# Optimization experiments

Hardware: AMD Instinct MI355X
Metric: run time of the kernel (lower is better)

## Reference

```python
import math
import jax, jax.numpy as jnp
from jax import lax
import numpy as np

D_MODEL, D_STATE, D_CONV, EXPAND = 96, 16, 3, 2
D_INNER = EXPAND * D_MODEL            # 192
DT_RANK = math.ceil(D_MODEL / 16)     # 6
B_, H_, W_ = 2, 64, 64


def setup_inputs() -> dict:
    key = jax.random.key(0)
    ks = jax.random.split(key, 8)
    x = jax.random.normal(ks[0], (B_, H_, W_, D_MODEL), jnp.float32)
    in_proj_w = jax.random.normal(ks[1], (2 * D_INNER, D_MODEL), jnp.float32) * (D_MODEL ** -0.5)
    conv_w = jax.random.normal(ks[2], (D_INNER, 1, D_CONV, D_CONV), jnp.float32) * 0.1  # depthwise OIHW
    conv_b = jax.random.normal(ks[3], (D_INNER,), jnp.float32) * 0.1
    x_proj_weight = jax.random.normal(ks[4], (4, DT_RANK + 2 * D_STATE, D_INNER), jnp.float32) * (D_INNER ** -0.5)
    dt_init_std = DT_RANK ** -0.5
    dt_projs_weight = jax.random.uniform(ks[5], (4, D_INNER, DT_RANK), jnp.float32, -dt_init_std, dt_init_std)
    dt = jnp.exp(jax.random.uniform(ks[6], (4, D_INNER), jnp.float32) * (math.log(0.1) - math.log(0.001)) + math.log(0.001))
    dt = jnp.clip(dt, 1e-4, None)
    dt_projs_bias = dt + jnp.log(-jnp.expm1(-dt))  # inverse softplus init
    A_logs = jnp.log(jnp.tile(jnp.arange(1.0, D_STATE + 1.0, dtype=jnp.float32), (4 * D_INNER, 1)))  # (4*D, N)
    Ds = jnp.ones((4 * D_INNER,), jnp.float32)
    out_norm_w = jnp.ones((D_INNER,), jnp.float32)
    out_norm_b = jnp.zeros((D_INNER,), jnp.float32)
    out_proj_w = jax.random.normal(ks[7], (D_MODEL, D_INNER), jnp.float32) * (D_INNER ** -0.5)
    return dict(x=x, in_proj_w=in_proj_w, conv_w=conv_w, conv_b=conv_b,
                x_proj_weight=x_proj_weight, dt_projs_weight=dt_projs_weight,
                dt_projs_bias=dt_projs_bias, A_logs=A_logs, Ds=Ds,
                out_norm_w=out_norm_w, out_norm_b=out_norm_b, out_proj_w=out_proj_w)


def _ss2d(x, in_proj_w, conv_w, conv_b, x_proj_weight, dt_projs_weight,
          dt_projs_bias, A_logs, Ds, out_norm_w, out_norm_b, out_proj_w):
    B, H, W, C = x.shape
    K = 4
    d_inner = conv_w.shape[0]
    d_state = A_logs.shape[1]
    dt_rank = dt_projs_weight.shape[2]
    L = H * W

    # in_proj + split into x / gate z
    xz = jnp.einsum('bhwc,ec->bhwe', x, in_proj_w)
    xi, z = jnp.split(xz, 2, axis=-1)

    # depthwise 3x3 conv (padding=1) + SiLU, channels-first
    xc = jnp.transpose(xi, (0, 3, 1, 2))  # B,D,H,W
    xc = lax.conv_general_dilated(xc, conv_w, (1, 1), 'SAME',
                                  feature_group_count=d_inner,
                                  dimension_numbers=('NCHW', 'OIHW', 'NCHW'))
    xc = jax.nn.silu(xc + conv_b[None, :, None, None])

    # 4 scan directions: row-major, col-major, and their reverses
    x_hw = xc.reshape(B, d_inner, L)
    x_wh = jnp.transpose(xc, (0, 1, 3, 2)).reshape(B, d_inner, L)
    x_hwwh = jnp.stack([x_hw, x_wh], axis=1)                        # B,2,D,L
    xs = jnp.concatenate([x_hwwh, jnp.flip(x_hwwh, axis=-1)], axis=1)  # B,K,D,L

    x_dbl = jnp.einsum('bkdl,kcd->bkcl', xs, x_proj_weight)
    dts, Bs, Cs = jnp.split(x_dbl, [dt_rank, dt_rank + d_state], axis=2)
    dts = jnp.einsum('bkrl,kdr->bkdl', dts, dt_projs_weight)
    delta = jax.nn.softplus(dts + dt_projs_bias[None, :, :, None])  # B,K,D,L
    A = -jnp.exp(A_logs).reshape(K, d_inner, d_state)               # K,D,N

    # selective scan over L (serial recurrence)
    d_s = jnp.moveaxis(delta, -1, 0)  # L,B,K,D
    u_s = jnp.moveaxis(xs, -1, 0)     # L,B,K,D
    B_s = jnp.moveaxis(Bs, -1, 0)     # L,B,K,N
    C_s = jnp.moveaxis(Cs, -1, 0)     # L,B,K,N

    def step(h, inp):
        d_t, u_t, Bt, Ct = inp
        dA = jnp.exp(d_t[..., None] * A)                       # B,K,D,N
        h = h * dA + (d_t * u_t)[..., None] * Bt[:, :, None, :]
        y = jnp.einsum('bkdn,bkn->bkd', h, Ct)
        return h, y

    h0 = jnp.zeros((B, K, d_inner, d_state), jnp.float32)
    _, ys = lax.scan(step, h0, (d_s, u_s, B_s, C_s))  # ys: L,B,K,D
    ys = jnp.moveaxis(ys, 0, -1)                      # B,K,D,L
    out_y = ys + xs * Ds.reshape(K, d_inner)[None, :, :, None]

    # merge directions back to row-major layout
    inv_y = jnp.flip(out_y[:, 2:4], axis=-1)
    wh_y = jnp.transpose(out_y[:, 1].reshape(B, d_inner, W, H), (0, 1, 3, 2)).reshape(B, d_inner, L)
    invwh_y = jnp.transpose(inv_y[:, 1].reshape(B, d_inner, W, H), (0, 1, 3, 2)).reshape(B, d_inner, L)
    y = out_y[:, 0] + inv_y[:, 0] + wh_y + invwh_y    # B,D,L

    y = jnp.transpose(y, (0, 2, 1)).reshape(B, H, W, d_inner)
    mu = y.mean(-1, keepdims=True)
    var = y.var(-1, keepdims=True)
    y = (y - mu) * lax.rsqrt(var + 1e-5) * out_norm_w + out_norm_b
    y = y * jax.nn.silu(z)
    return jnp.einsum('bhwd,cd->bhwc', y, out_proj_w)


def reference(x, in_proj_w, conv_w, conv_b, x_proj_weight, dt_projs_weight,
              dt_projs_bias, A_logs, Ds, out_norm_w, out_norm_b, out_proj_w):
    return _ss2d(x, in_proj_w, conv_w, conv_b, x_proj_weight, dt_projs_weight,
                 dt_projs_bias, A_logs, Ds, out_norm_w, out_norm_b, out_proj_w)
```

## Files before the change

### kernel.cpp

```cpp
#include <hip/hip_runtime.h>
#include <math.h>

#define DMODEL 96
#define DIN    192
#define NST    16
#define RK     6
#define KDIR   4
#define LLEN   4096
#define BB     2
#define BP_TOT 8192
#define SCH    128
#define TCH    32

__global__ __launch_bounds__(192) void k_inproj(const float* __restrict__ x,
                                                const float* __restrict__ Wp,
                                                float* __restrict__ xi,
                                                float* __restrict__ z)
{
    __shared__ float xs[8 * 96];
    const int t  = threadIdx.x;
    const int p0 = blockIdx.x * 8;
    for (int idx = t; idx < 768; idx += 192)
        xs[idx] = x[(size_t)p0 * 96 + idx];
    __syncthreads();

    float acc0[8], acc1[8];
    #pragma unroll
    for (int i = 0; i < 8; ++i) { acc0[i] = 0.f; acc1[i] = 0.f; }
    const float* w0p = Wp + (size_t)t * 96;
    const float* w1p = Wp + (size_t)(t + 192) * 96;
    for (int k = 0; k < 96; k += 4) {
        float4 w0 = *(const float4*)(w0p + k);
        float4 w1 = *(const float4*)(w1p + k);
        #pragma unroll
        for (int p = 0; p < 8; ++p) {
            float4 xv = *(const float4*)&xs[p * 96 + k];
            acc0[p] = fmaf(w0.x, xv.x, fmaf(w0.y, xv.y, fmaf(w0.z, xv.z, fmaf(w0.w, xv.w, acc0[p]))));
            acc1[p] = fmaf(w1.x, xv.x, fmaf(w1.y, xv.y, fmaf(w1.z, xv.z, fmaf(w1.w, xv.w, acc1[p]))));
        }
    }
    #pragma unroll
    for (int p = 0; p < 8; ++p) {
        xi[(size_t)(p0 + p) * 192 + t] = acc0[p];
        z [(size_t)(p0 + p) * 192 + t] = acc1[p];
    }
}

__global__ __launch_bounds__(256) void k_conv(const float* __restrict__ xi,
                                              const float* __restrict__ cw,
                                              const float* __restrict__ cb,
                                              float* __restrict__ xc)
{
    int tid = blockIdx.x * 256 + threadIdx.x;
    int d  = tid % 192;
    int bp = tid / 192;
    int p  = bp & 4095;
    int b  = bp >> 12;
    int h  = p >> 6, w = p & 63;
    float s = cb[d];
    #pragma unroll
    for (int ky = 0; ky < 3; ++ky) {
        int hh = h + ky - 1;
        if (hh < 0 || hh >= 64) continue;
        #pragma unroll
        for (int kx = 0; kx < 3; ++kx) {
            int ww = w + kx - 1;
            if (ww < 0 || ww >= 64) continue;
            s += xi[((size_t)b * 4096 + hh * 64 + ww) * 192 + d] * cw[d * 9 + ky * 3 + kx];
        }
    }
    xc[tid] = s * (1.f / (1.f + __expf(-s)));
}

__device__ __forceinline__ int inv_perm(int kd, int p)
{
    if (kd == 0) return p;
    if (kd == 1) return ((p & 63) << 6) | (p >> 6);
    if (kd == 2) return 4095 - p;
    return 4095 - (((p & 63) << 6) | (p >> 6));
}

__device__ __forceinline__ int perm_pos(int k, int l)
{
    if (k == 0) return l;
    if (k == 1) return ((l & 63) << 6) | (l >> 6);
    if (k == 2) return 4095 - l;
    int lr = 4095 - l;
    return ((lr & 63) << 6) | (lr >> 6);
}

__device__ __forceinline__ float softplus_fast(float x)
{
    float r = __logf(1.f + __expf(x));
    return (x > 15.f) ? x : r;
}

__device__ __forceinline__ void pow_chain(float e1, float* aa)
{
    float e2 = e1 * e1, e4 = e2 * e2, e8 = e4 * e4, e16 = e8 * e8;
    float e3 = e2 * e1, e5 = e4 * e1, e6 = e4 * e2, e7 = e4 * e3;
    aa[0] = e1;  aa[1] = e2;  aa[2] = e3;  aa[3] = e4;
    aa[4] = e5;  aa[5] = e6;  aa[6] = e7;  aa[7] = e8;
    aa[8] = e8 * e1;  aa[9] = e8 * e2;  aa[10] = e8 * e3;  aa[11] = e8 * e4;
    aa[12] = e8 * e5; aa[13] = e8 * e6; aa[14] = e8 * e7;  aa[15] = e16;
}

__device__ __forceinline__ int sm_remap(int c)
{
    return (c < 6) ? (32 + c) : (c - 6);
}

__global__ __launch_bounds__(192) void k_xdbl(const float* __restrict__ xc,
                                              const float* __restrict__ xpw,
                                              float* __restrict__ xdk,
                                              float* __restrict__ y)
{
    __shared__ float xs[8 * 192];
    const int t  = threadIdx.x;
    const int p0 = blockIdx.x * 8;
    for (int idx = t; idx < 1536; idx += 192) {
        xs[idx] = xc[(size_t)p0 * 192 + idx];
        y[(size_t)p0 * 192 + idx] = 0.f;
    }
    __syncthreads();
    if (t >= 152) return;

    const int kd = t / 38, r = t % 38;
    float acc[8];
    #pragma unroll
    for (int i = 0; i < 8; ++i) acc[i] = 0.f;
    const float* wr = xpw + (size_t)t * 192;
    for (int k = 0; k < 192; k += 4) {
        float4 w = *(const float4*)(wr + k);
        #pragma unroll
        for (int p = 0; p < 8; ++p) {
            float4 xv = *(const float4*)&xs[p * 192 + k];
            acc[p] = fmaf(w.x, xv.x, fmaf(w.y, xv.y, fmaf(w.z, xv.z, fmaf(w.w, xv.w, acc[p]))));
        }
    }
    #pragma unroll
    for (int p = 0; p < 8; ++p) {
        int bp = p0 + p;
        int b  = bp >> 12, pp = bp & 4095;
        int l  = inv_perm(kd, pp);
        xdk[((size_t)(b * 4 + kd) * 4096 + l) * 38 + r] = acc[p];
    }
}

__global__ __launch_bounds__(192) void k_scan1(const float* __restrict__ xc,
                                               const float* __restrict__ xdk,
                                               const float* __restrict__ dtw,
                                               const float* __restrict__ dtb,
                                               const float* __restrict__ Alog,
                                               const float* __restrict__ Ds,
                                               float* __restrict__ hend,
                                               float* __restrict__ prodA,
                                               float* __restrict__ cdbuf,
                                               float* __restrict__ y)
{
    __shared__ float sm[TCH * 40];
    const int t   = threadIdx.x;
    const int blk = blockIdx.x;
    const int s = blk & (SCH - 1), k = (blk >> 7) & 3, b = blk >> 9;
    const int kd = k * 192 + t;
    const int l0 = s * TCH;

    const float* src = xdk + ((size_t)(b * 4 + k) * 4096 + l0) * 38;
    for (int idx = t; idx < TCH * 38; idx += 192) {
        int st = idx / 38, c = idx % 38;
        sm[st * 40 + sm_remap(c)] = src[idx];
    }

    const float A0 = -__expf(Alog[kd * 16]);
    bool fast = true;
    #pragma unroll
    for (int n = 1; n < 16; ++n) {
        float An = -__expf(Alog[kd * 16 + n]);
        fast = fast && (fabsf(An - (float)(n + 1) * A0) <= 1e-3f * fabsf(An));
    }
    float wdt[6];
    #pragma unroll
    for (int r = 0; r < 6; ++r) wdt[r] = dtw[kd * 6 + r];
    const float bias = dtb[kd];
    const float Dk   = Ds[kd];

    float h[16];
    #pragma unroll
    for (int n = 0; n < 16; ++n) h[n] = 0.f;
    float cd = 0.f;

    const float* xcb = xc + (size_t)b * 4096 * 192;
    float* yb = y + (size_t)b * 4096 * 192;
    int allfast = __syncthreads_and((int)fast);

    int p_cur = perm_pos(k, l0);
    float u = xcb[(size_t)p_cur * 192 + t];

    if (allfast) {
        for (int st = 0; st < TCH; ++st) {
            int p_next = (st + 1 < TCH) ? perm_pos(k, l0 + st + 1) : p_cur;
            float u_next = xcb[(size_t)p_next * 192 + t];
            const float* r = &sm[st * 40];
            float4 dq = *(const float4*)(r + 32);
            float xv = bias + dq.x * wdt[0] + dq.y * wdt[1] + dq.z * wdt[2]
                            + dq.w * wdt[3] + r[36] * wdt[4] + r[37] * wdt[5];
            float delta = softplus_fast(xv);
            cd += delta;
            cdbuf[((size_t)blk * TCH + st) * 192 + t] = cd;
            float du = delta * u;
            float aa[16];
            pow_chain(__expf(delta * A0), aa);
            float4 b0 = *(const float4*)(r),      b1 = *(const float4*)(r + 4);
            float4 b2 = *(const float4*)(r + 8),  b3 = *(const float4*)(r + 12);
            float4 c0 = *(const float4*)(r + 16), c1 = *(const float4*)(r + 20);
            float4 c2 = *(const float4*)(r + 24), c3 = *(const float4*)(r + 28);
            float bv[16] = {b0.x, b0.y, b0.z, b0.w, b1.x, b1.y, b1.z, b1.w,
                            b2.x, b2.y, b2.z, b2.w, b3.x, b3.y, b3.z, b3.w};
            float cv[16] = {c0.x, c0.y, c0.z, c0.w, c1.x, c1.y, c1.z, c1.w,
                            c2.x, c2.y, c2.z, c2.w, c3.x, c3.y, c3.z, c3.w};
            float acc = Dk * u;
            #pragma unroll
            for (int n = 0; n < 16; ++n) {
                h[n] = fmaf(h[n], aa[n], du * bv[n]);
                acc  = fmaf(h[n], cv[n], acc);
            }
            unsafeAtomicAdd(&yb[(size_t)p_cur * 192 + t], acc);
            u = u_next; p_cur = p_next;
        }
    } else {
        for (int st = 0; st < TCH; ++st) {
            int p_next = (st + 1 < TCH) ? perm_pos(k, l0 + st + 1) : p_cur;
            float u_next = xcb[(size_t)p_next * 192 + t];
            const float* r = &sm[st * 40];
            float xv = bias;
            #pragma unroll
            for (int j = 0; j < 6; ++j) xv += r[32 + j] * wdt[j];
            float delta = softplus_fast(xv);
            cd += delta;
            float du = delta * u;
            #pragma unroll
            for (int n = 0; n < 16; ++n) {
                float An = -__expf(Alog[kd * 16 + n]);
                h[n] = fmaf(h[n], __expf(delta * An), du * r[n]);
            }
            u = u_next; p_cur = p_next;
        }
    }

    size_t base = (size_t)blk * 3072 + t * 16;
    float ap[16];
    if (allfast) {
        pow_chain(__expf(cd * A0), ap);
    } else {
        #pragma unroll
        for (int n = 0; n < 16; ++n)
            ap[n] = __expf(-__expf(Alog[kd * 16 + n]) * cd);
    }
    #pragma unroll
    for (int i = 0; i < 4; ++i) {
        *(float4*)&hend [base + 4 * i] = make_float4(h[4*i], h[4*i+1], h[4*i+2], h[4*i+3]);
        *(float4*)&prodA[base + 4 * i] = make_float4(ap[4*i], ap[4*i+1], ap[4*i+2], ap[4*i+3]);
    }
}

__global__ __launch_bounds__(256) void k_scan2(const float* __restrict__ hend,
                                               float* __restrict__ prodA)
{
    int tid = blockIdx.x * 256 + threadIdx.x;
    int n  = tid & 15;
    int d  = (tid >> 4) % 192;
    int bk = tid / (192 * 16);
    size_t base = (size_t)bk * SCH * 3072 + d * 16 + n;
    float carry = 0.f;
    for (int s = 0; s < SCH; ++s) {
        size_t a = base + (size_t)s * 3072;
        float pa = prodA[a];
        float he = hend[a];
        prodA[a] = carry;
        carry = fmaf(pa, carry, he);
    }
}

__global__ __launch_bounds__(192) void k_scan3(const float* __restrict__ xc,
                                               const float* __restrict__ xdk,
                                               const float* __restrict__ dtw,
                                               const float* __restrict__ dtb,
                                               const float* __restrict__ Alog,
                                               const float* __restrict__ Ds,
                                               const float* __restrict__ hinit,
                                               const float* __restrict__ cdbuf,
                                               float* __restrict__ y)
{
    __shared__ float sm[TCH * 40];
    const int t   = threadIdx.x;
    const int blk = blockIdx.x;
    const int s = blk & (SCH - 1), k = (blk >> 7) & 3, b = blk >> 9;
    const int kd = k * 192 + t;
    const int l0 = s * TCH;

    const float* src = xdk + ((size_t)(b * 4 + k) * 4096 + l0) * 38;
    float* yb = y + (size_t)b * 4096 * 192;

    const float A0 = -__expf(Alog[kd * 16]);
    bool fast = true;
    #pragma unroll
    for (int n = 1; n < 16; ++n) {
        float An = -__expf(Alog[kd * 16 + n]);
        fast = fast && (fabsf(An - (float)(n + 1) * A0) <= 1e-3f * fabsf(An));
    }
    int allfast = __syncthreads_and((int)fast);

    float hi[16];
    size_t hbase = (size_t)blk * 3072 + t * 16;
    #pragma unroll
    for (int i = 0; i < 4; ++i) {
        float4 v = *(const float4*)&hinit[hbase + 4 * i];
        hi[4*i] = v.x; hi[4*i+1] = v.y; hi[4*i+2] = v.z; hi[4*i+3] = v.w;
    }

    if (allfast) {
        if (s == 0) return;
        for (int idx = t; idx < TCH * 16; idx += 192) {
            int st = idx >> 4, c = idx & 15;
            sm[st * 16 + c] = src[st * 38 + 22 + c];
        }
        __syncthreads();
        const float* cdp = cdbuf + (size_t)blk * TCH * 192 + t;
        float cd_next = cdp[0];
        for (int st = 0; st < TCH; ++st) {
            float cdv = cd_next;
            if (st + 1 < TCH) cd_next = cdp[(size_t)(st + 1) * 192];
            float aa[16];
            pow_chain(__expf(cdv * A0), aa);
            const float* r = &sm[st * 16];
            float corr = 0.f;
            #pragma unroll
            for (int n = 0; n < 16; ++n)
                corr = fmaf(aa[n] * hi[n], r[n], corr);
            unsafeAtomicAdd(&yb[(size_t)perm_pos(k, l0 + st) * 192 + t], corr);
        }
    } else {
        for (int idx = t; idx < TCH * 38; idx += 192) {
            int st = idx / 38, c = idx % 38;
            sm[st * 40 + sm_remap(c)] = src[idx];
        }
        __syncthreads();
        const float* xcb = xc + (size_t)b * 4096 * 192;
        float wdt[6];
        #pragma unroll
        for (int r = 0; r < 6; ++r) wdt[r] = dtw[kd * 6 + r];
        const float bias = dtb[kd];
        const float Dk   = Ds[kd];
        float h[16];
        #pragma unroll
        for (int n = 0; n < 16; ++n) h[n] = hi[n];
        int p_cur = perm_pos(k, l0);
        float u = xcb[(size_t)p_cur * 192 + t];
        for (int st = 0; st < TCH; ++st) {
            int p_next = (st + 1 < TCH) ? perm_pos(k, l0 + st + 1) : p_cur;
            float u_next = xcb[(size_t)p_next * 192 + t];
            const float* r = &sm[st * 40];
            float xv = bias;
            #pragma unroll
            for (int j = 0; j < 6; ++j) xv += r[32 + j] * wdt[j];
            float delta = softplus_fast(xv);
            float du = delta * u;
            float acc = Dk * u;
            #pragma unroll
            for (int n = 0; n < 16; ++n) {
                float An = -__expf(Alog[kd * 16 + n]);
                h[n] = fmaf(h[n], __expf(delta * An), du * r[n]);
                acc  = fmaf(h[n], r[16 + n], acc);
            }
            unsafeAtomicAdd(&yb[(size_t)p_cur * 192 + t], acc);
            u = u_next; p_cur = p_next;
        }
    }
}

__global__ __launch_bounds__(192) void k_lnout(const float* __restrict__ y,
                                               const float* __restrict__ zb,
                                               const float* __restrict__ onw,
                                               const float* __restrict__ onb,
                                               const float* __restrict__ Wo,
                                               float* __restrict__ out)
{
    __shared__ float ys[1536];
    __shared__ float ps[192], pq[192];
    __shared__ float mu[8], ri[8];
    const int t  = threadIdx.x;
    const int p0 = blockIdx.x * 8;

    #pragma unroll
    for (int i = 0; i < 8; ++i)
        ys[i * 192 + t] = y[(size_t)p0 * 192 + i * 192 + t];
    __syncthreads();

    {
        int pg = t / 24, j = t % 24;
        float s1 = 0.f, s2 = 0.f;
        #pragma unroll
        for (int m = 0; m < 8; ++m) {
            float v = ys[pg * 192 + j + 24 * m];
            s1 += v; s2 += v * v;
        }
        ps[t] = s1; pq[t] = s2;
    }
    __syncthreads();
    if (t < 8) {
        float s1 = 0.f, s2 = 0.f;
        #pragma unroll
        for (int j = 0; j < 24; ++j) { s1 += ps[t * 24 + j]; s2 += pq[t * 24 + j]; }
        float mean = s1 * (1.f / 192.f);
        float var  = s2 * (1.f / 192.f) - mean * mean;
        mu[t] = mean;
        ri[t] = rsqrtf(var + 1e-5f);
    }
    __syncthreads();

    {
        float w = onw[t], bo = onb[t];
        #pragma unroll
        for (int i = 0; i < 8; ++i) {
            float v  = ys[i * 192 + t];
            float yn = (v - mu[i]) * ri[i] * w + bo;
            float zv = zb[(size_t)(p0 + i) * 192 + t];
            float sg = 1.f / (1.f + __expf(-zv));
            ys[i * 192 + t] = yn * (zv * sg);
        }
    }
    __syncthreads();

    const int pg = t / 96, c = t % 96;
    float acc[4];
    #pragma unroll
    for (int i = 0; i < 4; ++i) acc[i] = 0.f;
    const float* wr = Wo + (size_t)c * 192;
    for (int k = 0; k < 192; k += 4) {
        float4 w = *(const float4*)(wr + k);
        #pragma unroll
        for (int i = 0; i < 4; ++i) {
            float4 xv = *(const float4*)&ys[(pg * 4 + i) * 192 + k];
            acc[i] = fmaf(w.x, xv.x, fmaf(w.y, xv.y, fmaf(w.z, xv.z, fmaf(w.w, xv.w, acc[i]))));
        }
    }
    #pragma unroll
    for (int i = 0; i < 4; ++i)
        out[(size_t)(p0 + pg * 4 + i) * 96 + c] = acc[i];
}

extern "C" void kernel_launch(void* const* d_in, const int* in_sizes, int n_in,
                              void* d_out, int out_size, void* d_ws, size_t ws_size,
                              hipStream_t stream)
{
    const float* x    = (const float*)d_in[0];
    const float* Wp   = (const float*)d_in[1];
    const float* cw   = (const float*)d_in[2];
    const float* cb   = (const float*)d_in[3];
    const float* xpw  = (const float*)d_in[4];
    const float* dtw  = (const float*)d_in[5];
    const float* dtb  = (const float*)d_in[6];
    const float* Alog = (const float*)d_in[7];
    const float* Ds   = (const float*)d_in[8];
    const float* onw  = (const float*)d_in[9];
    const float* onb  = (const float*)d_in[10];
    const float* Wo   = (const float*)d_in[11];
    float* out = (float*)d_out;

    const size_t NBP  = (size_t)BP_TOT * 192;
    const size_t NXD  = (size_t)BB * 4 * 4096 * 38;
    const size_t NSC  = (size_t)BB * 4 * SCH * 3072;
    float* WS    = (float*)d_ws;
    float* xc    = WS;
    float* zb    = WS + NBP;
    float* xiy   = WS + 2 * NBP;
    float* xdk   = WS + 3 * NBP;
    float* hend  = xdk + NXD;
    float* prodA = hend + NSC;
    float* cdbuf = prodA + NSC;

    k_inproj<<<1024, 192, 0, stream>>>(x, Wp, xiy, zb);
    k_conv  <<<6144, 256, 0, stream>>>(xiy, cw, cb, xc);
    k_xdbl  <<<1024, 192, 0, stream>>>(xc, xpw, xdk, xiy);
    k_scan1 <<<1024, 192, 0, stream>>>(xc, xdk, dtw, dtb, Alog, Ds, hend, prodA, cdbuf, xiy);
    k_scan2 <<<96, 256, 0, stream>>>(hend, prodA);
    k_scan3 <<<1024, 192, 0, stream>>>(xc, xdk, dtw, dtb, Alog, Ds, prodA, cdbuf, xiy);
    k_lnout <<<1024, 192, 0, stream>>>(xiy, zb, onw, onb, Wo, out);
}
```

Before: 229.3 us.

## Fuse conv into x_proj, drop atomics via per-direction buffers, parallelize chunk scan

Merges the depthwise conv+SiLU into the x_proj kernel, with each thread loading a 3x10 register window and reusing it across 8 pixels. The scan kernels now write per-direction output buffers with plain stores instead of atomics, and k_lnout sums the four direction buffers. scan3 recomputes cumulative delta instead of reading a stored cdbuf, which removes that large write and read. scan2 becomes a two-level parallel scan over 1536 blocks instead of 96 serial threads-blocks, at the cost of a larger yk buffer and more reads in lnout.

New measurement: 210.3 us. 8.3% less time.

```diff
diff --git a/kernel.cpp b/kernel.cpp
--- a/kernel.cpp
+++ b/kernel.cpp
@@ -46,32 +46,6 @@
     }
 }
 
-__global__ __launch_bounds__(256) void k_conv(const float* __restrict__ xi,
-                                              const float* __restrict__ cw,
-                                              const float* __restrict__ cb,
-                                              float* __restrict__ xc)
-{
-    int tid = blockIdx.x * 256 + threadIdx.x;
-    int d  = tid % 192;
-    int bp = tid / 192;
-    int p  = bp & 4095;
-    int b  = bp >> 12;
-    int h  = p >> 6, w = p & 63;
-    float s = cb[d];
-    #pragma unroll
-    for (int ky = 0; ky < 3; ++ky) {
-        int hh = h + ky - 1;
-        if (hh < 0 || hh >= 64) continue;
-        #pragma unroll
-        for (int kx = 0; kx < 3; ++kx) {
-            int ww = w + kx - 1;
-            if (ww < 0 || ww >= 64) continue;
-            s += xi[((size_t)b * 4096 + hh * 64 + ww) * 192 + d] * cw[d * 9 + ky * 3 + kx];
-        }
-    }
-    xc[tid] = s * (1.f / (1.f + __expf(-s)));
-}
-
 __device__ __forceinline__ int inv_perm(int kd, int p)
 {
     if (kd == 0) return p;
@@ -110,17 +84,49 @@
     return (c < 6) ? (32 + c) : (c - 6);
 }
 
-__global__ __launch_bounds__(192) void k_xdbl(const float* __restrict__ xc,
-                                              const float* __restrict__ xpw,
-                                              float* __restrict__ xdk,
-                                              float* __restrict__ y)
+__global__ __launch_bounds__(192) void k_convxdbl(const float* __restrict__ xi,
+                                                  const float* __restrict__ cw,
+                                                  const float* __restrict__ cb,
+                                                  const float* __restrict__ xpw,
+                                                  float* __restrict__ xc,
+                                                  float* __restrict__ xdk)
 {
     __shared__ float xs[8 * 192];
-    const int t  = threadIdx.x;
-    const int p0 = blockIdx.x * 8;
-    for (int idx = t; idx < 1536; idx += 192) {
-        xs[idx] = xc[(size_t)p0 * 192 + idx];
-        y[(size_t)p0 * 192 + idx] = 0.f;
+    const int t   = threadIdx.x;
+    const int p0  = blockIdx.x * 8;
+    const int b   = p0 >> 12;
+    const int pp0 = p0 & 4095;
+    const int row = pp0 >> 6, c0 = pp0 & 63;
+
+    float w9[9];
+    #pragma unroll
+    for (int i = 0; i < 9; ++i) w9[i] = cw[t * 9 + i];
+    const float cbias = cb[t];
+
+    float xv[3][10];
+    #pragma unroll
+    for (int ky = 0; ky < 3; ++ky) {
+        int rr = row + ky - 1;
+        #pragma unroll
+        for (int kx = 0; kx < 10; ++kx) {
+            int cc = c0 + kx - 1;
+            float v = 0.f;
+            if (rr >= 0 && rr < 64 && cc >= 0 && cc < 64)
+                v = xi[((size_t)b * 4096 + rr * 64 + cc) * 192 + t];
+            xv[ky][kx] = v;
+        }
+    }
+    #pragma unroll
+    for (int p = 0; p < 8; ++p) {
+        float s = cbias;
+        #pragma unroll
+        for (int ky = 0; ky < 3; ++ky)
+            #pragma unroll
+            for (int kx = 0; kx < 3; ++kx)
+                s = fmaf(xv[ky][p + kx], w9[ky * 3 + kx], s);
+        float sv = s * (1.f / (1.f + __expf(-s)));
+        xc[(size_t)(p0 + p) * 192 + t] = sv;
+        xs[p * 192 + t] = sv;
     }
     __syncthreads();
     if (t >= 152) return;
@@ -134,14 +140,13 @@
         float4 w = *(const float4*)(wr + k);
         #pragma unroll
         for (int p = 0; p < 8; ++p) {
-            float4 xv = *(const float4*)&xs[p * 192 + k];
-            acc[p] = fmaf(w.x, xv.x, fmaf(w.y, xv.y, fmaf(w.z, xv.z, fmaf(w.w, xv.w, acc[p]))));
+            float4 x4 = *(const float4*)&xs[p * 192 + k];
+            acc[p] = fmaf(w.x, x4.x, fmaf(w.y, x4.y, fmaf(w.z, x4.z, fmaf(w.w, x4.w, acc[p]))));
         }
     }
     #pragma unroll
     for (int p = 0; p < 8; ++p) {
-        int bp = p0 + p;
-        int b  = bp >> 12, pp = bp & 4095;
+        int pp = pp0 + p;
         int l  = inv_perm(kd, pp);
         xdk[((size_t)(b * 4 + kd) * 4096 + l) * 38 + r] = acc[p];
     }
@@ -155,8 +160,7 @@
                                                const float* __restrict__ Ds,
                                                float* __restrict__ hend,
                                                float* __restrict__ prodA,
-                                               float* __restrict__ cdbuf,
-                                               float* __restrict__ y)
+                                               float* __restrict__ yk)
 {
     __shared__ float sm[TCH * 40];
     const int t   = threadIdx.x;
@@ -190,7 +194,7 @@
     float cd = 0.f;
 
     const float* xcb = xc + (size_t)b * 4096 * 192;
-    float* yb = y + (size_t)b * 4096 * 192;
+    float* ykb = yk + (size_t)(b * 4 + k) * 4096 * 192;
     int allfast = __syncthreads_and((int)fast);
 
     int p_cur = perm_pos(k, l0);
@@ -206,7 +210,6 @@
                             + dq.w * wdt[3] + r[36] * wdt[4] + r[37] * wdt[5];
             float delta = softplus_fast(xv);
             cd += delta;
-            cdbuf[((size_t)blk * TCH + st) * 192 + t] = cd;
             float du = delta * u;
             float aa[16];
             pow_chain(__expf(delta * A0), aa);
@@ -224,7 +227,7 @@
                 h[n] = fmaf(h[n], aa[n], du * bv[n]);
                 acc  = fmaf(h[n], cv[n], acc);
             }
-            unsafeAtomicAdd(&yb[(size_t)p_cur * 192 + t], acc);
+            ykb[(size_t)p_cur * 192 + t] = acc;
             u = u_next; p_cur = p_next;
         }
     } else {
@@ -266,18 +269,39 @@
 __global__ __launch_bounds__(256) void k_scan2(const float* __restrict__ hend,
                                                float* __restrict__ prodA)
 {
-    int tid = blockIdx.x * 256 + threadIdx.x;
-    int n  = tid & 15;
-    int d  = (tid >> 4) % 192;
-    int bk = tid / (192 * 16);
-    size_t base = (size_t)bk * SCH * 3072 + d * 16 + n;
-    float carry = 0.f;
-    for (int s = 0; s < SCH; ++s) {
-        size_t a = base + (size_t)s * 3072;
-        float pa = prodA[a];
-        float he = hend[a];
-        prodA[a] = carry;
-        carry = fmaf(pa, carry, he);
+    __shared__ float smA[256], smH[256];
+    const int t = threadIdx.x;
+    const int g = t >> 4, n = t & 15;
+    const int bk = blockIdx.x / 192, d = blockIdx.x % 192;
+    const size_t base = (size_t)bk * SCH * 3072 + d * 16 + n;
+
+    float a_[8], h_[8];
+    float A = 1.f, H = 0.f;
+    #pragma unroll
+    for (int i = 0; i < 8; ++i) {
+        size_t rec = base + (size_t)(g * 8 + i) * 3072;
+        a_[i] = prodA[rec];
+        h_[i] = hend[rec];
+        H = fmaf(a_[i], H, h_[i]);
+        A *= a_[i];
+    }
+    smA[t] = A; smH[t] = H;
+    __syncthreads();
+    if (t < 16) {
+        float carry = 0.f;
+        for (int g2 = 0; g2 < 16; ++g2) {
+            float ta = smA[g2 * 16 + t], th = smH[g2 * 16 + t];
+            smH[g2 * 16 + t] = carry;
+            carry = fmaf(ta, carry, th);
+        }
+    }
+    __syncthreads();
+    float carry = smH[t];
+    #pragma unroll
+    for (int i = 0; i < 8; ++i) {
+        size_t rec = base + (size_t)(g * 8 + i) * 3072;
+        prodA[rec] = carry;
+        carry = fmaf(a_[i], carry, h_[i]);
     }
 }
 
@@ -288,8 +312,7 @@
                                                const float* __restrict__ Alog,
                                                const float* __restrict__ Ds,
                                                const float* __restrict__ hinit,
-                                               const float* __restrict__ cdbuf,
-                                               float* __restrict__ y)
+                                               float* __restrict__ yk)
 {
     __shared__ float sm[TCH * 40];
     const int t   = threadIdx.x;
@@ -299,7 +322,7 @@
     const int l0 = s * TCH;
 
     const float* src = xdk + ((size_t)(b * 4 + k) * 4096 + l0) * 38;
-    float* yb = y + (size_t)b * 4096 * 192;
+    float* ykb = yk + (size_t)(b * 4 + k) * 4096 * 192;
 
     const float A0 = -__expf(Alog[kd * 16]);
     bool fast = true;
@@ -320,24 +343,30 @@
 
     if (allfast) {
         if (s == 0) return;
-        for (int idx = t; idx < TCH * 16; idx += 192) {
-            int st = idx >> 4, c = idx & 15;
-            sm[st * 16 + c] = src[st * 38 + 22 + c];
-        }
+        for (int idx = t; idx < TCH * 22; idx += 192) {
+            int st = idx / 22, c = idx % 22;
+            int gcol = (c < 6) ? c : (16 + c);
+            sm[st * 24 + ((c < 6) ? (16 + c) : (c - 6))] = src[st * 38 + gcol];
+        }
+        float wdt[6];
+        #pragma unroll
+        for (int r = 0; r < 6; ++r) wdt[r] = dtw[kd * 6 + r];
+        const float bias = dtb[kd];
         __syncthreads();
-        const float* cdp = cdbuf + (size_t)blk * TCH * 192 + t;
-        float cd_next = cdp[0];
+        float cd = 0.f;
         for (int st = 0; st < TCH; ++st) {
-            float cdv = cd_next;
-            if (st + 1 < TCH) cd_next = cdp[(size_t)(st + 1) * 192];
+            const float* r = &sm[st * 24];
+            float xv = bias + r[16] * wdt[0] + r[17] * wdt[1] + r[18] * wdt[2]
+                            + r[19] * wdt[3] + r[20] * wdt[4] + r[21] * wdt[5];
+            cd += softplus_fast(xv);
             float aa[16];
-            pow_chain(__expf(cdv * A0), aa);
-            const float* r = &sm[st * 16];
+            pow_chain(__expf(cd * A0), aa);
             float corr = 0.f;
             #pragma unroll
             for (int n = 0; n < 16; ++n)
                 corr = fmaf(aa[n] * hi[n], r[n], corr);
-            unsafeAtomicAdd(&yb[(size_t)perm_pos(k, l0 + st) * 192 + t], corr);
+            size_t off = (size_t)perm_pos(k, l0 + st) * 192 + t;
+            ykb[off] += corr;
         }
     } else {
         for (int idx = t; idx < TCH * 38; idx += 192) {
@@ -372,13 +401,13 @@
                 h[n] = fmaf(h[n], __expf(delta * An), du * r[n]);
                 acc  = fmaf(h[n], r[16 + n], acc);
             }
-            unsafeAtomicAdd(&yb[(size_t)p_cur * 192 + t], acc);
+            ykb[(size_t)p_cur * 192 + t] = acc;
             u = u_next; p_cur = p_next;
         }
     }
 }
 
-__global__ __launch_bounds__(192) void k_lnout(const float* __restrict__ y,
+__global__ __launch_bounds__(192) void k_lnout(const float* __restrict__ yk,
                                                const float* __restrict__ zb,
                                                const float* __restrict__ onw,
                                                const float* __restrict__ onb,
@@ -388,12 +417,17 @@
     __shared__ float ys[1536];
     __shared__ float ps[192], pq[192];
     __shared__ float mu[8], ri[8];
-    const int t  = threadIdx.x;
-    const int p0 = blockIdx.x * 8;
-
-    #pragma unroll
-    for (int i = 0; i < 8; ++i)
-        ys[i * 192 + t] = y[(size_t)p0 * 192 + i * 192 + t];
+    const int t   = threadIdx.x;
+    const int p0  = blockIdx.x * 8;
+    const int b   = p0 >> 12;
+    const int pp0 = p0 & 4095;
+    const size_t KSTR = (size_t)4096 * 192;
+
+    #pragma unroll
+    for (int i = 0; i < 8; ++i) {
+        size_t base = ((size_t)(b * 4) * 4096 + pp0 + i) * 192 + t;
+        ys[i * 192 + t] = yk[base] + yk[base + KSTR] + yk[base + 2 * KSTR] + yk[base + 3 * KSTR];
+    }
     __syncthreads();
 
     {
@@ -471,19 +505,18 @@
     const size_t NXD  = (size_t)BB * 4 * 4096 * 38;
     const size_t NSC  = (size_t)BB * 4 * SCH * 3072;
     float* WS    = (float*)d_ws;
-    float* xc    = WS;
+    float* xibuf = WS;
     float* zb    = WS + NBP;
-    float* xiy   = WS + 2 * NBP;
+    float* xc    = WS + 2 * NBP;
     float* xdk   = WS + 3 * NBP;
     float* hend  = xdk + NXD;
     float* prodA = hend + NSC;
-    float* cdbuf = prodA + NSC;
-
-    k_inproj<<<1024, 192, 0, stream>>>(x, Wp, xiy, zb);
-    k_conv  <<<6144, 256, 0, stream>>>(xiy, cw, cb, xc);
-    k_xdbl  <<<1024, 192, 0, stream>>>(xc, xpw, xdk, xiy);
-    k_scan1 <<<1024, 192, 0, stream>>>(xc, xdk, dtw, dtb, Alog, Ds, hend, prodA, cdbuf, xiy);
-    k_scan2 <<<96, 256, 0, stream>>>(hend, prodA);
-    k_scan3 <<<1024, 192, 0, stream>>>(xc, xdk, dtw, dtb, Alog, Ds, prodA, cdbuf, xiy);
-    k_lnout <<<1024, 192, 0, stream>>>(xiy, zb, onw, onb, Wo, out);
-}
+    float* yk    = prodA + NSC;
+
+    k_inproj  <<<1024, 192, 0, stream>>>(x, Wp, xibuf, zb);
+    k_convxdbl<<<1024, 192, 0, stream>>>(xibuf, cw, cb, xpw, xc, xdk);
+    k_scan1   <<<1024, 192, 0, stream>>>(xc, xdk, dtw, dtb, Alog, Ds, hend, prodA, yk);
+    k_scan2   <<<1536, 256, 0, stream>>>(hend, prodA);
+    k_scan3   <<<1024, 192, 0, stream>>>(xc, xdk, dtw, dtb, Alog, Ds, prodA, yk);
+    k_lnout   <<<1024, 192, 0, stream>>>(yk, zb, onw, onb, Wo, out);
+}
```
